# Kernel optimization log

Measured on AMD Instinct MI355X. Metric: run time of the kernel, lower is better.

Reference implementation:

```python
import jax, jax.numpy as jnp
import numpy as np

B, T, C, H, HS = 16, 512, 768, 12, 64  # head_size = d_model // n_head
EPS = 1e-5


def setup_inputs() -> dict:
    key = jax.random.key(0)
    ks = jax.random.split(key, 16)
    s = 0.02
    inp = {
        "x": jax.random.normal(ks[0], (B, T, C), jnp.float32),
        "norm_w": jnp.ones((C,), jnp.float32),
        # per-head stacked QKV projections (shared attention module, used twice)
        "Wq": jax.random.normal(ks[1], (H, C, HS), jnp.float32) * s,
        "bq": jnp.zeros((H, HS), jnp.float32),
        "Wk": jax.random.normal(ks[2], (H, C, HS), jnp.float32) * s,
        "bk": jnp.zeros((H, HS), jnp.float32),
        "Wv": jax.random.normal(ks[3], (H, C, HS), jnp.float32) * s,
        "bv": jnp.zeros((H, HS), jnp.float32),
        # learned relative-position bias table, per head: (H, T, T, HS)
        "rel_pos": jax.random.normal(ks[4], (H, T, T, HS), jnp.float32),
        "Wproj": jax.random.normal(ks[5], (C, C), jnp.float32) * s,
        "bproj": jnp.zeros((C,), jnp.float32),
        # FFN: Linear(C, 5C) -> GELU -> Linear(5C, C)
        "W1": jax.random.normal(ks[6], (C, 5 * C), jnp.float32) * s,
        "b1": jnp.zeros((5 * C,), jnp.float32),
        "W2": jax.random.normal(ks[7], (5 * C, C), jnp.float32) * s,
        "b2": jnp.zeros((C,), jnp.float32),
    }
    return inp


def _rmsnorm(x, w, eps=EPS):
    xf = x.astype(jnp.float32)
    n = xf * jax.lax.rsqrt(jnp.mean(xf * xf, axis=-1, keepdims=True) + eps)
    return n.astype(x.dtype) * w


def _attention(xn, Wq, bq, Wk, bk, Wv, bv, rel_pos, Wproj, bproj, masked):
    # xn: (B,T,C); per-head projections -> (B,H,T,HS)
    q = jnp.einsum('btc,hcd->bhtd', xn, Wq) + bq[None, :, None, :]
    k = jnp.einsum('btc,hcd->bhtd', xn, Wk) + bk[None, :, None, :]
    v = jnp.einsum('btc,hcd->bhtd', xn, Wv) + bv[None, :, None, :]
    # NOTE: source divides by head_size**(-0.5), i.e. MULTIPLIES by sqrt(HS).
    scores = jnp.einsum('bhtd,bhsd->bhts', q, k) * jnp.sqrt(jnp.float32(HS))
    if masked:
        tril = jnp.tril(jnp.ones((T, T), bool))
        scores = jnp.where(tril[None, None], scores, -jnp.inf)
    else:
        # relative-position bias: einsum('btc,tvc->btv') per head
        scores = scores + jnp.einsum('bhtd,htsd->bhts', q, rel_pos)
    att = jax.nn.softmax(scores, axis=-1)
    out = jnp.einsum('bhts,bhsd->bhtd', att, v)        # (B,H,T,HS)
    out = out.transpose(0, 2, 1, 3).reshape(B, T, C)    # concat heads
    return out @ Wproj + bproj


def reference(x, norm_w, Wq, bq, Wk, bk, Wv, bv, rel_pos, Wproj, bproj, W1, b1, W2, b2):
    # pass 1: causal-masked attention (shared weights)
    x1 = x + _attention(_rmsnorm(x, norm_w), Wq, bq, Wk, bk, Wv, bv, rel_pos, Wproj, bproj, True)
    # pass 2: unmasked attention with relative-position bias (same weights)
    x2 = x1 + _attention(_rmsnorm(x1, norm_w), Wq, bq, Wk, bk, Wv, bv, rel_pos, Wproj, bproj, False)
    # FFN: Linear -> exact GELU -> Linear (dropout = identity at eval)
    h = jax.nn.gelu(_rmsnorm(x2, norm_w) @ W1 + b1, approximate=False)
    return x2 + (h @ W2 + b2)
```

## Files before the change

### kernel.cpp

```cpp
#include <hip/hip_runtime.h>

#define B_ 16
#define T_ 512
#define C_ 768
#define H_ 12
#define HS_ 64
#define F_ 3840
#define MROWS (B_*T_)

typedef __attribute__((ext_vector_type(8))) _Float16 half8;
typedef __attribute__((ext_vector_type(4))) float f32x4;

__device__ inline half8 cvt8(const float* __restrict__ p){
    const float4 a = ((const float4*)p)[0];
    const float4 b = ((const float4*)p)[1];
    half8 h;
    h[0]=(_Float16)a.x; h[1]=(_Float16)a.y; h[2]=(_Float16)a.z; h[3]=(_Float16)a.w;
    h[4]=(_Float16)b.x; h[5]=(_Float16)b.y; h[6]=(_Float16)b.z; h[7]=(_Float16)b.w;
    return h;
}

__global__ __launch_bounds__(256) void wt_kernel(const float* __restrict__ src,
                                                 _Float16* __restrict__ dst,
                                                 const int K, const int N){
    const int idx = blockIdx.x*256 + threadIdx.x;
    if (idx >= K*N) return;
    const int k = idx / N, n = idx - k*N;
    dst[(size_t)n*K + k] = (_Float16)src[idx];
}

__global__ __launch_bounds__(256) void wqkv_kernel(const float* __restrict__ src,
                                                   _Float16* __restrict__ dst){
    const int idx = blockIdx.x*256 + threadIdx.x;
    if (idx >= H_*C_*HS_) return;
    const int d = idx & 63;
    const int c = (idx >> 6) % C_;
    const int h = idx / (C_*HS_);
    dst[(size_t)(h*HS_ + d)*C_ + c] = (_Float16)src[idx];
}

__global__ __launch_bounds__(256) void rms_kernel(const float* __restrict__ src,
                                                  const float* __restrict__ w,
                                                  _Float16* __restrict__ dst){
    const int row = blockIdx.x;
    const float* x = src + (size_t)row*C_;
    const int tid = threadIdx.x;
    float v0 = x[tid], v1 = x[tid+256], v2 = x[tid+512];
    float s = v0*v0 + v1*v1 + v2*v2;
    #pragma unroll
    for (int off=1; off<64; off<<=1) s += __shfl_xor(s, off, 64);
    __shared__ float red[4];
    if ((tid&63)==0) red[tid>>6] = s;
    __syncthreads();
    s = red[0]+red[1]+red[2]+red[3];
    const float r = rsqrtf(s*(1.0f/C_) + 1e-5f);
    _Float16* d = dst + (size_t)row*C_;
    d[tid]     = (_Float16)(v0*r*w[tid]);
    d[tid+256] = (_Float16)(v1*r*w[tid+256]);
    d[tid+512] = (_Float16)(v2*r*w[tid+512]);
}

template<int KD>
__global__ __launch_bounds__(256) void gemm_kernel(
    const _Float16* __restrict__ A, const _Float16* __restrict__ Bt,
    const int Ndim,
    const float* __restrict__ bias,
    const float* __restrict__ resid,
    float* __restrict__ outf, _Float16* __restrict__ outh,
    const int layout, const int gelu)
{
    const int wave = threadIdx.x >> 6, ln = threadIdx.x & 63;
    const int lm = ln & 15, lq = ln >> 4;
    const int m0 = blockIdx.x*64 + wave*16;
    const int n0 = blockIdx.y*64;
    const _Float16* Ap  = A  + (size_t)(m0+lm)*KD + lq*8;
    const _Float16* Bp0 = Bt + (size_t)(n0+lm)*KD + lq*8;
    f32x4 acc0={},acc1={},acc2={},acc3={};
    for (int k=0; k<KD; k+=32){
        half8 a  = *(const half8*)(Ap + k);
        half8 b0 = *(const half8*)(Bp0 + k);
        half8 b1 = *(const half8*)(Bp0 + (size_t)16*KD + k);
        half8 b2 = *(const half8*)(Bp0 + (size_t)32*KD + k);
        half8 b3 = *(const half8*)(Bp0 + (size_t)48*KD + k);
        acc0 = __builtin_amdgcn_mfma_f32_16x16x32_f16(a,b0,acc0,0,0,0);
        acc1 = __builtin_amdgcn_mfma_f32_16x16x32_f16(a,b1,acc1,0,0,0);
        acc2 = __builtin_amdgcn_mfma_f32_16x16x32_f16(a,b2,acc2,0,0,0);
        acc3 = __builtin_amdgcn_mfma_f32_16x16x32_f16(a,b3,acc3,0,0,0);
    }
    f32x4 accs[4] = {acc0,acc1,acc2,acc3};
    #pragma unroll
    for (int nf=0; nf<4; nf++){
        const int n = n0 + nf*16 + lm;
        const float bv = bias ? bias[n] : 0.0f;
        #pragma unroll
        for (int i=0;i<4;i++){
            const int m = m0 + lq*4 + i;
            float v = accs[nf][i] + bv;
            if (gelu) v = 0.5f*v*(1.0f + erff(v*0.70710678118f));
            if (resid) v += resid[(size_t)m*Ndim + n];
            size_t oidx;
            if (layout == 0) oidx = (size_t)m*Ndim + n;
            else {
                const int b = m >> 9, t = m & 511, h = n >> 6, d = n & 63;
                if (layout == 1) oidx = (((size_t)(b*H_+h))*T_ + t)*HS_ + d;
                else             oidx = (((size_t)(b*H_+h))*HS_ + d)*T_ + t;
            }
            if (outf) outf[oidx] = v;
            if (outh) outh[oidx] = (_Float16)v;
        }
    }
}

__global__ __launch_bounds__(256) void qk_kernel(const _Float16* __restrict__ qb,
                                                 const _Float16* __restrict__ kb,
                                                 float* __restrict__ S, const int causal)
{
    const int bh = blockIdx.x;
    const int t0 = blockIdx.y*16;
    const int wave = threadIdx.x>>6, ln = threadIdx.x&63;
    const int s0 = (blockIdx.z*4 + wave)*16;
    const int lm = ln&15, lq = ln>>4;
    float* Sbh = S + (size_t)bh*T_*T_;
    if (causal && s0 > t0){
        #pragma unroll
        for (int i=0;i<4;i++)
            Sbh[(size_t)(t0+lq*4+i)*T_ + s0+lm] = -1e30f;
        return;
    }
    const _Float16* qp = qb + ((size_t)bh*T_ + t0+lm)*HS_ + lq*8;
    const _Float16* kp = kb + ((size_t)bh*T_ + s0+lm)*HS_ + lq*8;
    f32x4 acc = {};
    acc = __builtin_amdgcn_mfma_f32_16x16x32_f16(*(const half8*)qp,      *(const half8*)kp,      acc,0,0,0);
    acc = __builtin_amdgcn_mfma_f32_16x16x32_f16(*(const half8*)(qp+32), *(const half8*)(kp+32), acc,0,0,0);
    #pragma unroll
    for (int i=0;i<4;i++){
        const int t = t0 + lq*4 + i, s = s0 + lm;
        float v = 8.0f*acc[i];
        const size_t idx = (size_t)t*T_ + s;
        if (causal){ if (s > t) v = -1e30f; Sbh[idx] = v; }
        else Sbh[idx] += v;
    }
}

__global__ __launch_bounds__(256) void relbias_kernel(const _Float16* __restrict__ qb,
                                                      const float* __restrict__ rel,
                                                      float* __restrict__ S)
{
    const int ht = blockIdx.x;
    const int h = ht >> 9, t = ht & 511;
    const int wave = threadIdx.x>>6, ln = threadIdx.x&63;
    const int s0 = (blockIdx.y*4 + wave)*16;
    const int lm = ln&15, lq = ln>>4;
    const _Float16* qp = qb + (((size_t)lm*H_ + h)*T_ + t)*HS_ + lq*8;
    const float*    rp = rel + (((size_t)h*T_ + t)*T_ + s0+lm)*HS_ + lq*8;
    half8 a0 = *(const half8*)qp;
    half8 a1 = *(const half8*)(qp+32);
    f32x4 acc = {};
    acc = __builtin_amdgcn_mfma_f32_16x16x32_f16(a0, cvt8(rp),    acc,0,0,0);
    acc = __builtin_amdgcn_mfma_f32_16x16x32_f16(a1, cvt8(rp+32), acc,0,0,0);
    #pragma unroll
    for (int i=0;i<4;i++){
        const int bb = lq*4 + i;
        S[(((size_t)bb*H_ + h)*T_ + t)*T_ + s0+lm] = acc[i];
    }
}

__global__ __launch_bounds__(256) void softmax_kernel(float* __restrict__ S){
    const size_t row = blockIdx.x;
    float* p = S + row*T_;
    const int tid = threadIdx.x;
    float v0 = p[tid], v1 = p[tid+256];
    float m = fmaxf(v0, v1);
    #pragma unroll
    for (int off=1; off<64; off<<=1) m = fmaxf(m, __shfl_xor(m, off, 64));
    __shared__ float red[4];
    if ((tid&63)==0) red[tid>>6] = m;
    __syncthreads();
    m = fmaxf(fmaxf(red[0],red[1]), fmaxf(red[2],red[3]));
    const float e0 = expf(v0 - m), e1 = expf(v1 - m);
    float s = e0 + e1;
    #pragma unroll
    for (int off=1; off<64; off<<=1) s += __shfl_xor(s, off, 64);
    __syncthreads();
    if ((tid&63)==0) red[tid>>6] = s;
    __syncthreads();
    s = red[0]+red[1]+red[2]+red[3];
    const float inv = 1.0f/s;
    _Float16* ph = (_Float16*)p;
    ph[tid]     = (_Float16)(e0*inv);
    ph[tid+256] = (_Float16)(e1*inv);
}

__global__ __launch_bounds__(256) void pv_kernel(const float* __restrict__ S,
                                                 const _Float16* __restrict__ vt,
                                                 _Float16* __restrict__ att){
    const int bh = blockIdx.x;
    const int b = bh / H_, h = bh % H_;
    const int t0 = blockIdx.y*16;
    const int wave = threadIdx.x>>6, ln = threadIdx.x&63;
    const int d0 = wave*16;
    const int lm = ln&15, lq = ln>>4;
    const _Float16* Pp = (const _Float16*)(S + ((size_t)bh*T_ + t0+lm)*T_) + lq*8;
    const _Float16* Vp = vt + ((size_t)bh*HS_ + d0+lm)*T_ + lq*8;
    f32x4 acc = {};
    for (int k=0;k<T_;k+=32){
        half8 a   = *(const half8*)(Pp + k);
        half8 bfr = *(const half8*)(Vp + k);
        acc = __builtin_amdgcn_mfma_f32_16x16x32_f16(a,bfr,acc,0,0,0);
    }
    #pragma unroll
    for (int i=0;i<4;i++){
        const int t = t0 + lq*4 + i;
        att[((size_t)b*T_ + t)*C_ + h*HS_ + d0+lm] = (_Float16)acc[i];
    }
}

extern "C" void kernel_launch(void* const* d_in, const int* in_sizes, int n_in,
                              void* d_out, int out_size, void* d_ws, size_t ws_size,
                              hipStream_t stream){
    const float* x     = (const float*)d_in[0];
    const float* normw = (const float*)d_in[1];
    const float* Wq    = (const float*)d_in[2];
    const float* bq    = (const float*)d_in[3];
    const float* Wk    = (const float*)d_in[4];
    const float* bk    = (const float*)d_in[5];
    const float* Wv    = (const float*)d_in[6];
    const float* bv    = (const float*)d_in[7];
    const float* rel   = (const float*)d_in[8];
    const float* Wp    = (const float*)d_in[9];
    const float* bp    = (const float*)d_in[10];
    const float* W1    = (const float*)d_in[11];
    const float* b1    = (const float*)d_in[12];
    const float* W2    = (const float*)d_in[13];
    const float* b2    = (const float*)d_in[14];
    float* out = (float*)d_out;

    char* ws = (char*)d_ws;
    size_t off = 0;
    auto alloc = [&](size_t bytes)->char* {
        char* p = ws + off; off += (bytes + 255) & ~(size_t)255; return p;
    };
    _Float16* btq = (_Float16*)alloc((size_t)C_*C_*2);
    _Float16* btk = (_Float16*)alloc((size_t)C_*C_*2);
    _Float16* btv = (_Float16*)alloc((size_t)C_*C_*2);
    _Float16* btp = (_Float16*)alloc((size_t)C_*C_*2);
    _Float16* bt1 = (_Float16*)alloc((size_t)C_*F_*2);
    _Float16* bt2 = (_Float16*)alloc((size_t)C_*F_*2);
    _Float16* xn  = (_Float16*)alloc((size_t)MROWS*C_*2);
    _Float16* qb  = (_Float16*)alloc((size_t)MROWS*C_*2);
    _Float16* kb  = (_Float16*)alloc((size_t)MROWS*C_*2);
    _Float16* vtb = (_Float16*)alloc((size_t)MROWS*C_*2);
    float*    S   = (float*)   alloc((size_t)B_*H_*T_*T_*4);
    _Float16* att = (_Float16*)alloc((size_t)MROWS*C_*2);
    float*    x1f = (float*)   alloc((size_t)MROWS*C_*4);
    _Float16* hbuf= (_Float16*)alloc((size_t)MROWS*F_*2);

    const dim3 blk(256);
    wqkv_kernel<<<dim3((H_*C_*HS_+255)/256), blk, 0, stream>>>(Wq, btq);
    wqkv_kernel<<<dim3((H_*C_*HS_+255)/256), blk, 0, stream>>>(Wk, btk);
    wqkv_kernel<<<dim3((H_*C_*HS_+255)/256), blk, 0, stream>>>(Wv, btv);
    wt_kernel<<<dim3((C_*C_+255)/256), blk, 0, stream>>>(Wp, btp, C_, C_);
    wt_kernel<<<dim3((C_*F_+255)/256), blk, 0, stream>>>(W1, bt1, C_, F_);
    wt_kernel<<<dim3((C_*F_+255)/256), blk, 0, stream>>>(W2, bt2, F_, C_);

    const dim3 g_gemm768(MROWS/64, C_/64);
    const dim3 g_qk(B_*H_, T_/16, T_/64);
    const dim3 g_pv(B_*H_, T_/16);

    rms_kernel<<<dim3(MROWS), blk, 0, stream>>>(x, normw, xn);
    gemm_kernel<C_><<<g_gemm768, blk, 0, stream>>>(xn, btq, C_, bq, nullptr, nullptr, qb, 1, 0);
    gemm_kernel<C_><<<g_gemm768, blk, 0, stream>>>(xn, btk, C_, bk, nullptr, nullptr, kb, 1, 0);
    gemm_kernel<C_><<<g_gemm768, blk, 0, stream>>>(xn, btv, C_, bv, nullptr, nullptr, vtb, 2, 0);
    qk_kernel<<<g_qk, blk, 0, stream>>>(qb, kb, S, 1);
    softmax_kernel<<<dim3(B_*H_*T_), blk, 0, stream>>>(S);
    pv_kernel<<<g_pv, blk, 0, stream>>>(S, vtb, att);
    gemm_kernel<C_><<<g_gemm768, blk, 0, stream>>>(att, btp, C_, bp, x, x1f, nullptr, 0, 0);

    rms_kernel<<<dim3(MROWS), blk, 0, stream>>>(x1f, normw, xn);
    gemm_kernel<C_><<<g_gemm768, blk, 0, stream>>>(xn, btq, C_, bq, nullptr, nullptr, qb, 1, 0);
    gemm_kernel<C_><<<g_gemm768, blk, 0, stream>>>(xn, btk, C_, bk, nullptr, nullptr, kb, 1, 0);
    gemm_kernel<C_><<<g_gemm768, blk, 0, stream>>>(xn, btv, C_, bv, nullptr, nullptr, vtb, 2, 0);
    relbias_kernel<<<dim3(H_*T_, T_/64), blk, 0, stream>>>(qb, rel, S);
    qk_kernel<<<g_qk, blk, 0, stream>>>(qb, kb, S, 0);
    softmax_kernel<<<dim3(B_*H_*T_), blk, 0, stream>>>(S);
    pv_kernel<<<g_pv, blk, 0, stream>>>(S, vtb, att);
    gemm_kernel<C_><<<g_gemm768, blk, 0, stream>>>(att, btp, C_, bp, x1f, out, nullptr, 0, 0);

    rms_kernel<<<dim3(MROWS), blk, 0, stream>>>(out, normw, xn);
    gemm_kernel<C_><<<dim3(MROWS/64, F_/64), blk, 0, stream>>>(xn, bt1, F_, b1, nullptr, nullptr, hbuf, 0, 1);
    gemm_kernel<F_><<<g_gemm768, blk, 0, stream>>>(hbuf, bt2, C_, b2, out, out, nullptr, 0, 0);
}
```

Measured before the change: 3.204 ms.

## Fuse QK, softmax and PV into a flash-style online-softmax attention kernel

Replaces the separate QK score, softmax and PV kernels with one kernel that streams K/V tiles, keeps a running max and sum, and accumulates the output in registers. This avoids writing and re-reading the full B*H*T*T fp32 score matrix for the causal pass, and the causal pass now skips fully masked tiles. The relative-bias pass still materializes S through relbias_kernel but reads it only once inside the fused kernel. The cost is more register pressure and shuffles per tile, and K/V are loaded straight from global memory with no LDS reuse.

Result: faster. 2.873 ms (-10.3%).

```diff
diff --git a/kernel.cpp b/kernel.cpp
--- a/kernel.cpp
+++ b/kernel.cpp
@@ -111,37 +111,6 @@
     }
 }
 
-__global__ __launch_bounds__(256) void qk_kernel(const _Float16* __restrict__ qb,
-                                                 const _Float16* __restrict__ kb,
-                                                 float* __restrict__ S, const int causal)
-{
-    const int bh = blockIdx.x;
-    const int t0 = blockIdx.y*16;
-    const int wave = threadIdx.x>>6, ln = threadIdx.x&63;
-    const int s0 = (blockIdx.z*4 + wave)*16;
-    const int lm = ln&15, lq = ln>>4;
-    float* Sbh = S + (size_t)bh*T_*T_;
-    if (causal && s0 > t0){
-        #pragma unroll
-        for (int i=0;i<4;i++)
-            Sbh[(size_t)(t0+lq*4+i)*T_ + s0+lm] = -1e30f;
-        return;
-    }
-    const _Float16* qp = qb + ((size_t)bh*T_ + t0+lm)*HS_ + lq*8;
-    const _Float16* kp = kb + ((size_t)bh*T_ + s0+lm)*HS_ + lq*8;
-    f32x4 acc = {};
-    acc = __builtin_amdgcn_mfma_f32_16x16x32_f16(*(const half8*)qp,      *(const half8*)kp,      acc,0,0,0);
-    acc = __builtin_amdgcn_mfma_f32_16x16x32_f16(*(const half8*)(qp+32), *(const half8*)(kp+32), acc,0,0,0);
-    #pragma unroll
-    for (int i=0;i<4;i++){
-        const int t = t0 + lq*4 + i, s = s0 + lm;
-        float v = 8.0f*acc[i];
-        const size_t idx = (size_t)t*T_ + s;
-        if (causal){ if (s > t) v = -1e30f; Sbh[idx] = v; }
-        else Sbh[idx] += v;
-    }
-}
-
 __global__ __launch_bounds__(256) void relbias_kernel(const _Float16* __restrict__ qb,
                                                       const float* __restrict__ rel,
                                                       float* __restrict__ S)
@@ -165,53 +134,118 @@
     }
 }
 
-__global__ __launch_bounds__(256) void softmax_kernel(float* __restrict__ S){
-    const size_t row = blockIdx.x;
-    float* p = S + row*T_;
-    const int tid = threadIdx.x;
-    float v0 = p[tid], v1 = p[tid+256];
-    float m = fmaxf(v0, v1);
-    #pragma unroll
-    for (int off=1; off<64; off<<=1) m = fmaxf(m, __shfl_xor(m, off, 64));
-    __shared__ float red[4];
-    if ((tid&63)==0) red[tid>>6] = m;
-    __syncthreads();
-    m = fmaxf(fmaxf(red[0],red[1]), fmaxf(red[2],red[3]));
-    const float e0 = expf(v0 - m), e1 = expf(v1 - m);
-    float s = e0 + e1;
-    #pragma unroll
-    for (int off=1; off<64; off<<=1) s += __shfl_xor(s, off, 64);
-    __syncthreads();
-    if ((tid&63)==0) red[tid>>6] = s;
-    __syncthreads();
-    s = red[0]+red[1]+red[2]+red[3];
-    const float inv = 1.0f/s;
-    _Float16* ph = (_Float16*)p;
-    ph[tid]     = (_Float16)(e0*inv);
-    ph[tid+256] = (_Float16)(e1*inv);
-}
-
-__global__ __launch_bounds__(256) void pv_kernel(const float* __restrict__ S,
-                                                 const _Float16* __restrict__ vt,
-                                                 _Float16* __restrict__ att){
+__device__ inline unsigned pk2h(float a, float b){
+    union { _Float16 h[2]; unsigned u; } c;
+    c.h[0] = (_Float16)a; c.h[1] = (_Float16)b;
+    return c.u;
+}
+
+template<int CAUSAL>
+__global__ __launch_bounds__(256) void flash_kernel(
+    const _Float16* __restrict__ qb,
+    const _Float16* __restrict__ kb,
+    const _Float16* __restrict__ vt,
+    const float* __restrict__ bias,
+    _Float16* __restrict__ att)
+{
     const int bh = blockIdx.x;
-    const int b = bh / H_, h = bh % H_;
-    const int t0 = blockIdx.y*16;
-    const int wave = threadIdx.x>>6, ln = threadIdx.x&63;
-    const int d0 = wave*16;
-    const int lm = ln&15, lq = ln>>4;
-    const _Float16* Pp = (const _Float16*)(S + ((size_t)bh*T_ + t0+lm)*T_) + lq*8;
-    const _Float16* Vp = vt + ((size_t)bh*HS_ + d0+lm)*T_ + lq*8;
-    f32x4 acc = {};
-    for (int k=0;k<T_;k+=32){
-        half8 a   = *(const half8*)(Pp + k);
-        half8 bfr = *(const half8*)(Vp + k);
-        acc = __builtin_amdgcn_mfma_f32_16x16x32_f16(a,bfr,acc,0,0,0);
-    }
+    const int b = bh / H_, h = bh - b*H_;
+    const int wave = threadIdx.x >> 6, ln = threadIdx.x & 63;
+    const int lm = ln & 15, lq = ln >> 4;
+    const int t0 = blockIdx.y*64 + wave*16;
+
+    const _Float16* qp = qb + ((size_t)bh*T_ + t0 + lm)*HS_ + lq*8;
+    const half8 q0 = *(const half8*)qp;
+    const half8 q1 = *(const half8*)(qp + 32);
+    const _Float16* kbase = kb + ((size_t)bh*T_ + lm)*HS_ + lq*8;
+    const _Float16* vbase = vt + ((size_t)bh*HS_ + lm)*T_ + lq*8;
+    const float*    bp    = CAUSAL ? (const float*)nullptr
+                                   : bias + ((size_t)bh*T_ + t0 + lm)*T_ + lq*4;
+
+    f32x4 o0={},o1={},o2={},o3={};
+    float m_run = -1e30f, l_run = 0.0f;
+    const int send = CAUSAL ? (t0 + 16) : T_;
+
+    for (int s0 = 0; s0 < send; s0 += 32){
+        const _Float16* kp = kbase + (size_t)s0*HS_;
+        f32x4 a0={}, a1={};
+        a0 = __builtin_amdgcn_mfma_f32_16x16x32_f16(*(const half8*)kp,             q0, a0,0,0,0);
+        a0 = __builtin_amdgcn_mfma_f32_16x16x32_f16(*(const half8*)(kp+32),        q1, a0,0,0,0);
+        a1 = __builtin_amdgcn_mfma_f32_16x16x32_f16(*(const half8*)(kp+16*HS_),    q0, a1,0,0,0);
+        a1 = __builtin_amdgcn_mfma_f32_16x16x32_f16(*(const half8*)(kp+16*HS_+32), q1, a1,0,0,0);
+
+        f32x4 v0, v1;
+        if (CAUSAL){
+            const int t = t0 + lm;
+            #pragma unroll
+            for (int i=0;i<4;i++){
+                const int sA = s0 + lq*4 + i;
+                v0[i] = (sA      > t) ? -1e30f : 8.0f*a0[i];
+                v1[i] = (sA + 16 > t) ? -1e30f : 8.0f*a1[i];
+            }
+        } else {
+            const float4 bA = *(const float4*)(bp + s0);
+            const float4 bB = *(const float4*)(bp + s0 + 16);
+            v0[0]=fmaf(8.0f,a0[0],bA.x); v0[1]=fmaf(8.0f,a0[1],bA.y);
+            v0[2]=fmaf(8.0f,a0[2],bA.z); v0[3]=fmaf(8.0f,a0[3],bA.w);
+            v1[0]=fmaf(8.0f,a1[0],bB.x); v1[1]=fmaf(8.0f,a1[1],bB.y);
+            v1[2]=fmaf(8.0f,a1[2],bB.z); v1[3]=fmaf(8.0f,a1[3],bB.w);
+        }
+
+        float tm = fmaxf(fmaxf(fmaxf(v0[0],v0[1]),fmaxf(v0[2],v0[3])),
+                         fmaxf(fmaxf(v1[0],v1[1]),fmaxf(v1[2],v1[3])));
+        tm = fmaxf(tm, __shfl_xor(tm, 16, 64));
+        tm = fmaxf(tm, __shfl_xor(tm, 32, 64));
+        if (!__all(tm <= m_run)){
+            const float mnew = fmaxf(m_run, tm);
+            const float f = __expf(m_run - mnew);
+            m_run = mnew; l_run *= f;
+            #pragma unroll
+            for (int i=0;i<4;i++){
+                const float fi = __shfl(f, lq*4 + i, 64);
+                o0[i]*=fi; o1[i]*=fi; o2[i]*=fi; o3[i]*=fi;
+            }
+        }
+
+        f32x4 p0, p1;
+        #pragma unroll
+        for (int i=0;i<4;i++){ p0[i]=__expf(v0[i]-m_run); p1[i]=__expf(v1[i]-m_run); }
+        l_run += (p0[0]+p0[1]) + (p0[2]+p0[3]) + ((p1[0]+p1[1]) + (p1[2]+p1[3]));
+
+        const unsigned h01a = pk2h(p0[0],p0[1]), h23a = pk2h(p0[2],p0[3]);
+        const unsigned h01b = pk2h(p1[0],p1[1]), h23b = pk2h(p1[2],p1[3]);
+        const int srcA = (lq&1)*32 + lm, srcB = srcA + 16;
+        const unsigned s01a = __shfl(h01a, srcA, 64), s01b = __shfl(h01b, srcA, 64);
+        const unsigned s23a = __shfl(h23a, srcA, 64), s23b = __shfl(h23b, srcA, 64);
+        const unsigned u01a = __shfl(h01a, srcB, 64), u01b = __shfl(h01b, srcB, 64);
+        const unsigned u23a = __shfl(h23a, srcB, 64), u23b = __shfl(h23b, srcB, 64);
+        const bool hi = (lq >= 2);
+        uint4 aw;
+        aw.x = hi ? s01b : s01a;
+        aw.y = hi ? s23b : s23a;
+        aw.z = hi ? u01b : u01a;
+        aw.w = hi ? u23b : u23a;
+        const half8 pa = __builtin_bit_cast(half8, aw);
+
+        const _Float16* vp = vbase + s0;
+        o0 = __builtin_amdgcn_mfma_f32_16x16x32_f16(pa, *(const half8*)vp,            o0,0,0,0);
+        o1 = __builtin_amdgcn_mfma_f32_16x16x32_f16(pa, *(const half8*)(vp + 16*T_),  o1,0,0,0);
+        o2 = __builtin_amdgcn_mfma_f32_16x16x32_f16(pa, *(const half8*)(vp + 32*T_),  o2,0,0,0);
+        o3 = __builtin_amdgcn_mfma_f32_16x16x32_f16(pa, *(const half8*)(vp + 48*T_),  o3,0,0,0);
+    }
+
+    l_run += __shfl_xor(l_run, 16, 64);
+    l_run += __shfl_xor(l_run, 32, 64);
+    const float inv = 1.0f / l_run;
+    _Float16* op = att + ((size_t)b*T_ + t0)*C_ + h*HS_ + lm;
     #pragma unroll
     for (int i=0;i<4;i++){
-        const int t = t0 + lq*4 + i;
-        att[((size_t)b*T_ + t)*C_ + h*HS_ + d0+lm] = (_Float16)acc[i];
+        const float fi = __shfl(inv, lq*4 + i, 64);
+        _Float16* orow = op + (size_t)(lq*4 + i)*C_;
+        orow[0]  = (_Float16)(o0[i]*fi);
+        orow[16] = (_Float16)(o1[i]*fi);
+        orow[32] = (_Float16)(o2[i]*fi);
+        orow[48] = (_Float16)(o3[i]*fi);
     }
 }
 
@@ -264,16 +298,13 @@
     wt_kernel<<<dim3((C_*F_+255)/256), blk, 0, stream>>>(W2, bt2, F_, C_);
 
     const dim3 g_gemm768(MROWS/64, C_/64);
-    const dim3 g_qk(B_*H_, T_/16, T_/64);
-    const dim3 g_pv(B_*H_, T_/16);
+    const dim3 g_flash(B_*H_, T_/64);
 
     rms_kernel<<<dim3(MROWS), blk, 0, stream>>>(x, normw, xn);
     gemm_kernel<C_><<<g_gemm768, blk, 0, stream>>>(xn, btq, C_, bq, nullptr, nullptr, qb, 1, 0);
     gemm_kernel<C_><<<g_gemm768, blk, 0, stream>>>(xn, btk, C_, bk, nullptr, nullptr, kb, 1, 0);
     gemm_kernel<C_><<<g_gemm768, blk, 0, stream>>>(xn, btv, C_, bv, nullptr, nullptr, vtb, 2, 0);
-    qk_kernel<<<g_qk, blk, 0, stream>>>(qb, kb, S, 1);
-    softmax_kernel<<<dim3(B_*H_*T_), blk, 0, stream>>>(S);
-    pv_kernel<<<g_pv, blk, 0, stream>>>(S, vtb, att);
+    flash_kernel<1><<<g_flash, blk, 0, stream>>>(qb, kb, vtb, nullptr, att);
     gemm_kernel<C_><<<g_gemm768, blk, 0, stream>>>(att, btp, C_, bp, x, x1f, nullptr, 0, 0);
 
     rms_kernel<<<dim3(MROWS), blk, 0, stream>>>(x1f, normw, xn);
@@ -281,9 +312,7 @@
     gemm_kernel<C_><<<g_gemm768, blk, 0, stream>>>(xn, btk, C_, bk, nullptr, nullptr, kb, 1, 0);
     gemm_kernel<C_><<<g_gemm768, blk, 0, stream>>>(xn, btv, C_, bv, nullptr, nullptr, vtb, 2, 0);
     relbias_kernel<<<dim3(H_*T_, T_/64), blk, 0, stream>>>(qb, rel, S);
-    qk_kernel<<<g_qk, blk, 0, stream>>>(qb, kb, S, 0);
-    softmax_kernel<<<dim3(B_*H_*T_), blk, 0, stream>>>(S);
-    pv_kernel<<<g_pv, blk, 0, stream>>>(S, vtb, att);
+    flash_kernel<0><<<g_flash, blk, 0, stream>>>(qb, kb, vtb, S, att);
     gemm_kernel<C_><<<g_gemm768, blk, 0, stream>>>(att, btp, C_, bp, x1f, out, nullptr, 0, 0);
 
     rms_kernel<<<dim3(MROWS), blk, 0, stream>>>(out, normw, xn);
```
